# Kernel optimization log

Hardware: AMD Instinct MI355X
Metric: run time of the kernel (lower is better)

## Reference

```python
import jax, jax.numpy as jnp
import numpy as np
import math

IN_FEATURES = 512
RFF_FEATURES = 2048
OUT_FEATURES = 1000
N = 8192
RIDGE_PENALTY = 1.0
MEAN_FIELD_FACTOR = 25.0
RFF_SCALAR = math.sqrt(RFF_FEATURES / 2)  # 32.0


def _random_ortho(key, n, m):
    q, _ = jnp.linalg.qr(jax.random.normal(key, (n, m), dtype=jnp.float32))
    return q


def setup_inputs() -> dict:
    key = jax.random.key(0)
    k_d, k_w, k_norm, k_b, k_lw, k_lb, k_cov = jax.random.split(key, 7)
    D = jax.random.normal(k_d, (N, IN_FEATURES), dtype=jnp.float32)
    # RFF weight: concat of random orthonormal blocks (rff_features > in_features)
    ws = []
    dim_left = RFF_FEATURES
    kk = k_w
    while dim_left > IN_FEATURES:
        kk, sub = jax.random.split(kk)
        ws.append(_random_ortho(sub, IN_FEATURES, IN_FEATURES))
        dim_left -= IN_FEATURES
    kk, sub = jax.random.split(kk)
    ws.append(_random_ortho(sub, IN_FEATURES, dim_left))
    W = jnp.concatenate(ws, axis=1)  # [in, rff]
    feature_norm = jax.random.normal(k_norm, W.shape, dtype=jnp.float32) ** 2
    W = W * jnp.sqrt(feature_norm.sum(0))
    b = jax.random.uniform(k_b, (RFF_FEATURES,), dtype=jnp.float32) * (2.0 * math.pi)
    # logit head (nn.Linear): weight [out, rff], bias [out]
    bound = 1.0 / math.sqrt(RFF_FEATURES)
    logit_w = jax.random.uniform(k_lw, (OUT_FEATURES, RFF_FEATURES), dtype=jnp.float32,
                                 minval=-bound, maxval=bound)
    logit_b = jax.random.uniform(k_lb, (OUT_FEATURES,), dtype=jnp.float32,
                                 minval=-bound, maxval=bound)
    # positive-definite covariance buffer (stand-in for inverted precision)
    A = jax.random.normal(k_cov, (RFF_FEATURES, RFF_FEATURES), dtype=jnp.float32) * 0.01
    covariance = A @ A.T + jnp.eye(RFF_FEATURES, dtype=jnp.float32)
    return {"D": D, "W": W, "b": b, "logit_w": logit_w, "logit_b": logit_b,
            "covariance": covariance}


def reference(D, W, b, logit_w, logit_b, covariance):
    # RFF feature map: cos(D @ W + b) / rff_scalar  -> [N, rff]
    Phi = jnp.cos(D @ W + b) / RFF_SCALAR
    # linear head -> [N, out]
    pred = Phi @ logit_w.T + logit_b
    # diag(Phi @ cov @ Phi.T) * ridge computed row-wise in O(N*r^2)
    diag_cov = jnp.sum((Phi @ covariance) * Phi, axis=-1) * RIDGE_PENALTY  # [N]
    logits_scale = jnp.sqrt(1.0 + diag_cov * MEAN_FIELD_FACTOR)
    return pred / logits_scale[:, None]
```

## Files before the change

### kernel.cpp

```cpp
#include <hip/hip_runtime.h>
#include <hip/hip_fp8.h>
#include <math.h>

#define N_ROWS 8192
#define IN_F   512
#define RFF    2048
#define OUT_F  1000
#define OUT_PAD 1024
#define INV_RFF_SCALAR 0.03125f
#define MEAN_FIELD 25.0f
#define PHI_NT 24
#define PRED_NT 32

typedef __attribute__((ext_vector_type(8))) short short8;
typedef __attribute__((ext_vector_type(4))) float f32x4;
typedef __attribute__((ext_vector_type(2))) long long2v;

__device__ __forceinline__ unsigned short f32_to_bf16(float f) {
    unsigned u = __float_as_uint(f);
    unsigned r = 0x7FFFu + ((u >> 16) & 1u);
    return (unsigned short)((u + r) >> 16);
}
__device__ __forceinline__ float bf16_to_f32(unsigned short h) {
    return __uint_as_float(((unsigned)h) << 16);
}
__device__ __forceinline__ unsigned char f32_to_fp8(float x) {
    __hip_fp8_e4m3 q(x);
    return (unsigned char)q.__x;
}

__device__ __forceinline__ int perm64(int k) {
    return (k & ~63) | (((k >> 3) & 3) << 4) | (((k >> 5) & 1) << 3) | (k & 7);
}

__device__ __forceinline__ void stage_tile8(const unsigned char* __restrict__ X,
                                            int r0, int k0b, unsigned char* lds,
                                            int w, int lane) {
    #pragma unroll
    for (int h = 0; h < 4; ++h) {
        int qb = h * 256 + w * 64;
        int q = qb + lane;
        int rt = q >> 7, c = (q >> 4) & 7, r = q & 15;
        const void* g = X + (size_t)(r0 + rt * 16 + r) * RFF + k0b + c * 16;
        __builtin_amdgcn_global_load_lds(
            (const __attribute__((address_space(1))) void*)g,
            (__attribute__((address_space(3))) void*)(lds + qb * 16),
            16, 0, 0);
    }
}

__global__ __launch_bounds__(256) void conv_split_kernel(
    const float* __restrict__ X, unsigned short* __restrict__ H,
    unsigned short* __restrict__ L, int n4)
{
    int i = blockIdx.x * 256 + threadIdx.x;
    if (i >= n4) return;
    float4 v = ((const float4*)X)[i];
    ushort4 h, l;
    h.x = f32_to_bf16(v.x); l.x = f32_to_bf16(v.x - bf16_to_f32(h.x));
    h.y = f32_to_bf16(v.y); l.y = f32_to_bf16(v.y - bf16_to_f32(h.y));
    h.z = f32_to_bf16(v.z); l.z = f32_to_bf16(v.z - bf16_to_f32(h.z));
    h.w = f32_to_bf16(v.w); l.w = f32_to_bf16(v.w - bf16_to_f32(h.w));
    ((ushort4*)H)[i] = h;
    ((ushort4*)L)[i] = l;
}

__global__ __launch_bounds__(256) void conv_covu8_kernel(
    const float* __restrict__ X, unsigned char* __restrict__ O)
{
    int i = blockIdx.x * 256 + threadIdx.x;
    int base = i * 4;
    int row = base >> 11;
    int col = base & 2047;
    int bn = row >> 7, bk = col >> 7;
    float w = (bk < bn) ? 16.0f : (bk == bn ? 8.0f : 0.0f);
    float4 v = ((const float4*)X)[i];
    float w0 = (col + 0 == row) ? 0.0f : w;
    float w1 = (col + 1 == row) ? 0.0f : w;
    float w2 = (col + 2 == row) ? 0.0f : w;
    float w3 = (col + 3 == row) ? 0.0f : w;
    uchar4 o;
    o.x = f32_to_fp8(v.x * w0); o.y = f32_to_fp8(v.y * w1);
    o.z = f32_to_fp8(v.z * w2); o.w = f32_to_fp8(v.w * w3);
    *(uchar4*)(O + (size_t)row * RFF + perm64(col)) = o;
}

__global__ __launch_bounds__(256) void conv_covd_kernel(
    const float* __restrict__ X, float* __restrict__ Cd)
{
    int i = blockIdx.x * 256 + threadIdx.x;
    if (i < RFF) Cd[i] = X[(size_t)i * RFF + i];
}

__global__ __launch_bounds__(256) void conv_phi8_kernel(
    const unsigned short* __restrict__ Phi16, unsigned char* __restrict__ Phi8)
{
    int i = blockIdx.x * 256 + threadIdx.x;
    int base = i * 4;
    int row = base >> 11;
    int col = base & 2047;
    ushort4 v = ((const ushort4*)Phi16)[i];
    uchar4 o;
    o.x = f32_to_fp8(bf16_to_f32(v.x) * 32.0f);
    o.y = f32_to_fp8(bf16_to_f32(v.y) * 32.0f);
    o.z = f32_to_fp8(bf16_to_f32(v.z) * 32.0f);
    o.w = f32_to_fp8(bf16_to_f32(v.w) * 32.0f);
    *(uchar4*)(Phi8 + (size_t)row * RFF + perm64(col)) = o;
}

__global__ __launch_bounds__(256) void conv_lw_kernel(
    const float* __restrict__ Lw, unsigned short* __restrict__ O)
{
    int i = blockIdx.x * 256 + threadIdx.x;
    int base = i * 4;
    int row = base >> 11;
    ushort4 o;
    if (row < OUT_F) {
        float4 v = ((const float4*)Lw)[i];
        o.x = f32_to_bf16(v.x); o.y = f32_to_bf16(v.y);
        o.z = f32_to_bf16(v.z); o.w = f32_to_bf16(v.w);
    } else {
        o.x = o.y = o.z = o.w = 0;
    }
    ((ushort4*)O)[i] = o;
}

__global__ __launch_bounds__(256) void conv_wt_kernel(
    const float* __restrict__ W, unsigned short* __restrict__ TH,
    unsigned short* __restrict__ TL)
{
    __shared__ float tile[64][65];
    const int tid = threadIdx.x;
    const int n0 = blockIdx.x * 64;
    const int k0 = blockIdx.y * 64;
    #pragma unroll
    for (int i = 0; i < 16; ++i) {
        int e = i * 256 + tid;
        int r = e >> 6, c = e & 63;
        tile[r][c] = W[(size_t)(k0 + r) * RFF + n0 + c];
    }
    __syncthreads();
    #pragma unroll
    for (int i = 0; i < 16; ++i) {
        int e = i * 256 + tid;
        int r = e >> 6, c = e & 63;
        float v = tile[c][r];
        unsigned short h = f32_to_bf16(v);
        unsigned short l = f32_to_bf16(v - bf16_to_f32(h));
        TH[(size_t)(n0 + r) * IN_F + k0 + c] = h;
        TL[(size_t)(n0 + r) * IN_F + k0 + c] = l;
    }
}


__device__ __forceinline__ void gload16u(const void* g, unsigned short* lds) {
    __builtin_amdgcn_global_load_lds(
        (const __attribute__((address_space(1))) void*)g,
        (__attribute__((address_space(3))) void*)lds, 16, 0, 0);
}

__device__ __forceinline__ void stage_ab(const unsigned short* __restrict__ src,
                                         int stride, int r0v, int kk,
                                         unsigned short* ldsbuf,
                                         int Qa, int h, int w, int lane) {
    int q   = w * 64 + lane;
    int RT  = h * 8 + Qa * 4 + (q >> 7);
    int c   = (q >> 4) & 7, r = q & 15;
    const void* g = src + (size_t)(r0v + RT * 16 + r) * stride + kk + c * 8;
    int RTu = h * 8 + Qa * 4 + (w >> 1);
    int cu  = (w & 1) * 4;
    gload16u(g, ldsbuf + RTu * 1024 + cu * 128);
}

__device__ __forceinline__ void stageB_g(const unsigned short* __restrict__ src,
                                         int cc0, int kk, unsigned short* ldsbuf,
                                         int nh, int h, int w, int lane) {
    int q    = w * 64 + lane;
    int i    = q >> 7;
    int RTp  = (i >> 1) * 4 + nh * 2 + (i & 1);
    int c    = (q >> 4) & 7, r = q & 15;
    const void* g = src + (size_t)(cc0 + h * 128 + RTp * 16 + r) * IN_F + kk + c * 8;
    int iu   = w >> 1;
    int RTpu = (iu >> 1) * 4 + nh * 2 + (iu & 1);
    int RTu  = h * 8 + RTpu;
    int cu   = (w & 1) * 4;
    gload16u(g, ldsbuf + RTu * 1024 + cu * 128);
}

#define SB0() __builtin_amdgcn_sched_barrier(0)
#define BARRIER() do { SB0(); __builtin_amdgcn_s_barrier(); SB0(); } while (0)
#define WAITVM(N) do { asm volatile("s_waitcnt vmcnt(" #N ")"); SB0(); } while (0)


#define READ_FA(FA, mh) do {                                                  \
    _Pragma("unroll")                                                         \
    for (int i_ = 0; i_ < 4; ++i_) {                                          \
        FA[i_][0] = *(const short8*)(A + (wm * 8 + (mh) * 4 + i_) * 1024      \
                                       + quad * 128 + ln * 8);                \
        FA[i_][1] = *(const short8*)(A + (wm * 8 + (mh) * 4 + i_) * 1024      \
                                       + 512 + quad * 128 + ln * 8);          \
    } } while (0)

#define READ_FB(FB, nh) do {                                                  \
    _Pragma("unroll")                                                         \
    for (int j_ = 0; j_ < 2; ++j_) {                                          \
        FB[j_][0] = *(const short8*)(B + (wn * 4 + (nh) * 2 + j_) * 1024      \
                                       + quad * 128 + ln * 8);                \
        FB[j_][1] = *(const short8*)(B + (wn * 4 + (nh) * 2 + j_) * 1024      \
                                       + 512 + quad * 128 + ln * 8);          \
    } } while (0)

#define MFMA16(MH, NH, FA, FB) do {                                           \
    __builtin_amdgcn_s_setprio(1);                                            \
    _Pragma("unroll")                                                         \
    for (int s_ = 0; s_ < 2; ++s_)                                            \
        _Pragma("unroll")                                                     \
        for (int i_ = 0; i_ < 4; ++i_)                                        \
            _Pragma("unroll")                                                 \
            for (int j_ = 0; j_ < 2; ++j_)                                    \
                acc[(MH) * 4 + i_][(NH) * 2 + j_] =                           \
                    __builtin_amdgcn_mfma_f32_16x16x32_bf16(                  \
                        FA[i_][s_], FB[j_][s_],                               \
                        acc[(MH) * 4 + i_][(NH) * 2 + j_], 0, 0, 0);          \
    __builtin_amdgcn_s_setprio(0);                                            \
} while (0)

__global__ __launch_bounds__(512, 2) void phi_mfma8p_kernel(
    const unsigned short* __restrict__ Dh, const unsigned short* __restrict__ Dl,
    const unsigned short* __restrict__ Wth, const unsigned short* __restrict__ Wtl,
    const float* __restrict__ bias, unsigned short* __restrict__ Phi)
{
    __shared__ unsigned short ldsA[2 * 16384];
    __shared__ unsigned short ldsB[2 * 16384];
    const int tid = threadIdx.x;
    const int w = tid >> 6, lane = tid & 63;
    const int wm = w >> 2, wn = w & 3;
    const int quad = lane >> 4, ln = lane & 15;

    const int bid = blockIdx.x;
    const int xcd = bid & 7, idx = bid >> 3;
    const int rb = (xcd >> 1) * 8 + (idx & 7);
    const int cb = (xcd & 1) * 4 + (idx >> 3);
    const int r0 = rb * 256;
    const int c0 = cb * 256;

    f32x4 acc[8][4];
    #pragma unroll
    for (int i = 0; i < 8; ++i)
        #pragma unroll
        for (int j = 0; j < 4; ++j)
            acc[i][j] = (f32x4)(0.0f);

    stage_ab(Dh, IN_F, r0, 0, ldsA, 0, 0, w, lane);
    stage_ab(Dh, IN_F, r0, 0, ldsA, 0, 1, w, lane);
    stage_ab(Dh, IN_F, r0, 0, ldsA, 1, 0, w, lane);
    stage_ab(Dh, IN_F, r0, 0, ldsA, 1, 1, w, lane);
    stageB_g(Wth, c0, 0, ldsB, 0, 0, w, lane);
    stageB_g(Wth, c0, 0, ldsB, 0, 1, w, lane);
    stageB_g(Wth, c0, 0, ldsB, 1, 0, w, lane);
    stageB_g(Wth, c0, 0, ldsB, 1, 1, w, lane);
    stage_ab(Dh, IN_F, r0, 64, ldsA + 16384, 0, 0, w, lane);
    stage_ab(Dh, IN_F, r0, 64, ldsA + 16384, 0, 1, w, lane);
    stageB_g(Wth, c0, 64, ldsB + 16384, 0, 0, w, lane);
    stageB_g(Wth, c0, 64, ldsB + 16384, 0, 1, w, lane);
    WAITVM(4);
    BARRIER();

    for (int t = 0; t < PHI_NT - 1; ++t) {
        const int buf = t & 1;
        const unsigned short* A = ldsA + buf * 16384;
        const unsigned short* B = ldsB + buf * 16384;
        unsigned short* curA = ldsA + buf * 16384;
        unsigned short* curB = ldsB + buf * 16384;
        unsigned short* othA = ldsA + (buf ^ 1) * 16384;
        unsigned short* othB = ldsB + (buf ^ 1) * 16384;
        const bool has2 = (t + 2) < PHI_NT;
        const int k1 = (t + 1) * 64, k2 = (t + 2) * 64;
        const int kk1 = k1 & 511, kk2 = k2 & 511;
        const unsigned short* A1 = (k1 >= 1024) ? Dl : Dh;
        const unsigned short* B1 = (k1 >= 1024) ? Wth : (k1 >= 512 ? Wtl : Wth);
        const unsigned short* A2 = (k2 >= 1024) ? Dl : Dh;
        const unsigned short* B2 = (k2 >= 1024) ? Wth : (k2 >= 512 ? Wtl : Wth);

        short8 fa[4][2], fb0[2][2], fb1[2][2];

        READ_FA(fa, 0);
        READ_FB(fb0, 0);
        stage_ab(A1, IN_F, r0, kk1, othA, 1, 0, w, lane);
        stage_ab(A1, IN_F, r0, kk1, othA, 1, 1, w, lane);
        BARRIER();
        MFMA16(0, 0, fa, fb0);
        BARRIER();

        READ_FB(fb1, 1);
        stageB_g(B1, c0, kk1, othB, 1, 0, w, lane);
        stageB_g(B1, c0, kk1, othB, 1, 1, w, lane);
        BARRIER();
        MFMA16(0, 1, fa, fb1);
        BARRIER();

        READ_FA(fa, 1);
        if (has2) { stage_ab(A2, IN_F, r0, kk2, curA, 0, 0, w, lane);
                    stage_ab(A2, IN_F, r0, kk2, curA, 0, 1, w, lane); }
        BARRIER();
        MFMA16(1, 0, fa, fb0);
        BARRIER();

        if (has2) { stageB_g(B2, c0, kk2, curB, 0, 0, w, lane);
                    stageB_g(B2, c0, kk2, curB, 0, 1, w, lane);
                    WAITVM(4); }
        else      { WAITVM(0); }
        BARRIER();
        MFMA16(1, 1, fa, fb1);
        BARRIER();
    }

    {
        asm volatile("" ::: "memory");
        const unsigned short* A = ldsA + ((PHI_NT - 1) & 1) * 16384;
        const unsigned short* B = ldsB + ((PHI_NT - 1) & 1) * 16384;
        short8 fa[4][2], fb0[2][2], fb1[2][2];
        READ_FA(fa, 0);
        READ_FB(fb0, 0);
        READ_FB(fb1, 1);
        MFMA16(0, 0, fa, fb0);
        MFMA16(0, 1, fa, fb1);
        READ_FA(fa, 1);
        MFMA16(1, 0, fa, fb0);
        MFMA16(1, 1, fa, fb1);
    }

    float bv[4];
    #pragma unroll
    for (int nt = 0; nt < 4; ++nt)
        bv[nt] = bias[c0 + wn * 64 + nt * 16 + ln];
    #pragma unroll
    for (int mt = 0; mt < 8; ++mt)
        #pragma unroll
        for (int nt = 0; nt < 4; ++nt) {
            int col = c0 + wn * 64 + nt * 16 + ln;
            #pragma unroll
            for (int reg = 0; reg < 4; ++reg) {
                int row = r0 + wm * 128 + mt * 16 + quad * 4 + reg;
                float z = acc[mt][nt][reg] + bv[nt];
                float p = __cosf(z) * INV_RFF_SCALAR;
                Phi[(size_t)row * RFF + col] = f32_to_bf16(p);
            }
        }
}

__global__ __launch_bounds__(256, 2) void diag8_kernel(
    const unsigned char* __restrict__ Phi8, const unsigned char* __restrict__ CovU8,
    const unsigned short* __restrict__ Phi16, const float* __restrict__ Cd,
    float* __restrict__ diag)
{
    __shared__ __align__(16) unsigned char ldsA[2 * 16384];
    __shared__ __align__(16) unsigned char ldsB[2 * 16384];
    const int tid = threadIdx.x;
    const int w = tid >> 6, lane = tid & 63;
    const int wm = w >> 1, wn = w & 1;
    const int quad = lane >> 4, ln = lane & 15;
    const int J = 15 - blockIdx.x;
    const int r0 = blockIdx.y * 128;
    const int c0 = J * 128;
    const int kmax = (J + 1) * 128;

    f32x4 acc[4][4];
    #pragma unroll
    for (int i = 0; i < 4; ++i)
        #pragma unroll
        for (int j = 0; j < 4; ++j)
            acc[i][j] = (f32x4)(0.0f);

    stage_tile8(Phi8,  r0, 0, ldsA, w, lane);
    stage_tile8(CovU8, c0, 0, ldsB, w, lane);
    WAITVM(0);
    BARRIER();

    int it = 0;
    for (int k0 = 0; k0 < kmax; k0 += 128, ++it) {
        const int buf = it & 1;
        const unsigned char* A = ldsA + buf * 16384;
        const unsigned char* B = ldsB + buf * 16384;

        if (k0 + 128 < kmax) {
            stage_tile8(Phi8,  r0, k0 + 128, ldsA + (buf ^ 1) * 16384, w, lane);
            stage_tile8(CovU8, c0, k0 + 128, ldsB + (buf ^ 1) * 16384, w, lane);
        }

        __builtin_amdgcn_s_setprio(1);
        #pragma unroll
        for (int kb = 0; kb < 2; ++kb) {
            long2v fa[4], fb[4];
            #pragma unroll
            for (int t = 0; t < 4; ++t) {
                fa[t] = *(const long2v*)(A + (((wm * 4 + t) * 128 + (kb * 4 + quad) * 16 + ln) << 4));
                fb[t] = *(const long2v*)(B + (((wn * 4 + t) * 128 + (kb * 4 + quad) * 16 + ln) << 4));
            }
            #pragma unroll
            for (int mt = 0; mt < 4; ++mt)
                #pragma unroll
                for (int nt = 0; nt < 4; ++nt)
                    acc[mt][nt] = __builtin_amdgcn_mfma_f32_16x16x32_fp8_fp8(
                        fa[mt].x, fb[nt].x, acc[mt][nt], 0, 0, 0);
            #pragma unroll
            for (int mt = 0; mt < 4; ++mt)
                #pragma unroll
                for (int nt = 0; nt < 4; ++nt)
                    acc[mt][nt] = __builtin_amdgcn_mfma_f32_16x16x32_fp8_fp8(
                        fa[mt].y, fb[nt].y, acc[mt][nt], 0, 0, 0);
        }
        __builtin_amdgcn_s_setprio(0);

        WAITVM(0);
        BARRIER();
    }

    float cd[4];
    #pragma unroll
    for (int nt = 0; nt < 4; ++nt)
        cd[nt] = 256.0f * Cd[c0 + wn * 64 + nt * 16 + ln];
    #pragma unroll
    for (int mt = 0; mt < 4; ++mt) {
        float psum[4] = {0.f, 0.f, 0.f, 0.f};
        #pragma unroll
        for (int nt = 0; nt < 4; ++nt) {
            int col = c0 + wn * 64 + nt * 16 + ln;
            #pragma unroll
            for (int reg = 0; reg < 4; ++reg) {
                int row = r0 + wm * 64 + mt * 16 + quad * 4 + reg;
                float pv = bf16_to_f32(Phi16[(size_t)row * RFF + col]);
                psum[reg] = fmaf(fmaf(cd[nt], pv, acc[mt][nt][reg]), pv, psum[reg]);
            }
        }
        #pragma unroll
        for (int off = 1; off < 16; off <<= 1)
            #pragma unroll
            for (int reg = 0; reg < 4; ++reg)
                psum[reg] += __shfl_xor(psum[reg], off, 16);
        if (ln == 0) {
            #pragma unroll
            for (int reg = 0; reg < 4; ++reg) {
                int row = r0 + wm * 64 + mt * 16 + quad * 4 + reg;
                atomicAdd(&diag[row], psum[reg] * (1.0f / 256.0f));
            }
        }
    }
}

__global__ __launch_bounds__(512, 2) void pred_min2_kernel(
    const unsigned short* __restrict__ Phi, const unsigned short* __restrict__ Lw,
    const float* __restrict__ Lb, const float* __restrict__ diag,
    float* __restrict__ out)
{
    __shared__ unsigned short ldsA[2 * 16384];
    __shared__ unsigned short ldsB[2 * 8192];
    const int tid = threadIdx.x;
    const int w = tid >> 6, lane = tid & 63;
    const int wm = w >> 1, wn = w & 1;
    const int quad = lane >> 4, ln = lane & 15;

    const int bid = blockIdx.x;
    const int xcd = bid & 7, idx = bid >> 3;
    const int rb = xcd * 4 + (idx >> 3);
    const int cb = idx & 7;
    const int r0 = rb * 256;
    const int c0 = cb * 128;

    f32x4 acc[4][4];
    #pragma unroll
    for (int i = 0; i < 4; ++i)
        #pragma unroll
        for (int j = 0; j < 4; ++j)
            acc[i][j] = (f32x4)(0.0f);

    stage_ab(Phi, RFF, r0, 0, ldsA, 0, 0, w, lane);
    stage_ab(Phi, RFF, r0, 0, ldsA, 1, 0, w, lane);
    stage_ab(Phi, RFF, r0, 0, ldsA, 0, 1, w, lane);
    stage_ab(Phi, RFF, r0, 0, ldsA, 1, 1, w, lane);
    stage_ab(Lw,  RFF, c0, 0, ldsB, 0, 0, w, lane);
    stage_ab(Lw,  RFF, c0, 0, ldsB, 1, 0, w, lane);
    WAITVM(0);
    BARRIER();

    for (int t = 0; t < PRED_NT; ++t) {
        const int buf = t & 1;
        const unsigned short* A = ldsA + buf * 16384;
        const unsigned short* B = ldsB + buf * 8192;

        if (t + 1 < PRED_NT) {
            const int kk = (t + 1) * 64;
            unsigned short* nA = ldsA + (buf ^ 1) * 16384;
            unsigned short* nB = ldsB + (buf ^ 1) * 8192;
            stage_ab(Phi, RFF, r0, kk, nA, 0, 0, w, lane);
            stage_ab(Phi, RFF, r0, kk, nA, 1, 0, w, lane);
            stage_ab(Phi, RFF, r0, kk, nA, 0, 1, w, lane);
            stage_ab(Phi, RFF, r0, kk, nA, 1, 1, w, lane);
            stage_ab(Lw,  RFF, c0, kk, nB, 0, 0, w, lane);
            stage_ab(Lw,  RFF, c0, kk, nB, 1, 0, w, lane);
        }

        short8 fa[4][2], fb[4][2];
        #pragma unroll
        for (int i_ = 0; i_ < 4; ++i_) {
            fa[i_][0] = *(const short8*)(A + (wm * 4 + i_) * 1024 + quad * 128 + ln * 8);
            fa[i_][1] = *(const short8*)(A + (wm * 4 + i_) * 1024 + 512 + quad * 128 + ln * 8);
        }
        #pragma unroll
        for (int j_ = 0; j_ < 4; ++j_) {
            fb[j_][0] = *(const short8*)(B + (wn * 4 + j_) * 1024 + quad * 128 + ln * 8);
            fb[j_][1] = *(const short8*)(B + (wn * 4 + j_) * 1024 + 512 + quad * 128 + ln * 8);
        }
        __builtin_amdgcn_s_setprio(1);
        #pragma unroll
        for (int s_ = 0; s_ < 2; ++s_)
            #pragma unroll
            for (int i_ = 0; i_ < 4; ++i_)
                #pragma unroll
                for (int j_ = 0; j_ < 4; ++j_)
                    acc[i_][j_] = __builtin_amdgcn_mfma_f32_16x16x32_bf16(
                        fa[i_][s_], fb[j_][s_], acc[i_][j_], 0, 0, 0);
        __builtin_amdgcn_s_setprio(0);

        WAITVM(0);
        BARRIER();
    }

    #pragma unroll
    for (int mt = 0; mt < 4; ++mt) {
        float s[4];
        #pragma unroll
        for (int reg = 0; reg < 4; ++reg) {
            int row = r0 + wm * 64 + mt * 16 + quad * 4 + reg;
            s[reg] = 1.0f / sqrtf(1.0f + MEAN_FIELD * diag[row]);
        }
        #pragma unroll
        for (int nt = 0; nt < 4; ++nt) {
            int col = c0 + wn * 64 + nt * 16 + ln;
            if (col < OUT_F) {
                float bv = Lb[col];
                #pragma unroll
                for (int reg = 0; reg < 4; ++reg) {
                    int row = r0 + wm * 64 + mt * 16 + quad * 4 + reg;
                    out[(size_t)row * OUT_F + col] = (acc[mt][nt][reg] + bv) * s[reg];
                }
            }
        }
    }
}

extern "C" void kernel_launch(void* const* d_in, const int* in_sizes, int n_in,
                              void* d_out, int out_size, void* d_ws, size_t ws_size,
                              hipStream_t stream) {
    const float* D    = (const float*)d_in[0];
    const float* W    = (const float*)d_in[1];
    const float* bias = (const float*)d_in[2];
    const float* Lw   = (const float*)d_in[3];
    const float* Lb   = (const float*)d_in[4];
    const float* cov  = (const float*)d_in[5];
    float* out = (float*)d_out;

    char* p = (char*)d_ws;
    unsigned short* Phi16 = (unsigned short*)p;  p += (size_t)N_ROWS * RFF * 2;
    unsigned char*  Phi8  = (unsigned char*)p;
    unsigned short* Dh    = (unsigned short*)p;  p += (size_t)N_ROWS * IN_F * 2;
    unsigned short* Dl    = (unsigned short*)p;  p += (size_t)N_ROWS * IN_F * 2;
    unsigned short* Wth   = (unsigned short*)p;  p += (size_t)RFF * IN_F * 2;
    unsigned short* Wtl   = (unsigned short*)p;  p += (size_t)RFF * IN_F * 2;
    unsigned short* Lw16  = (unsigned short*)p;  p += (size_t)OUT_PAD * RFF * 2;
    unsigned char*  CovU8 = (unsigned char*)p;
    float*          Cd    = (float*)(p + (size_t)RFF * RFF);
    p += (size_t)RFF * RFF * 2;
    float* diag           = (float*)p;

    hipMemsetAsync(diag, 0, N_ROWS * sizeof(float), stream);

    dim3 blk(256);
    conv_split_kernel<<<dim3((N_ROWS * IN_F / 4 + 255) / 256), blk, 0, stream>>>(D, Dh, Dl, N_ROWS * IN_F / 4);
    conv_wt_kernel<<<dim3(RFF / 64, IN_F / 64), blk, 0, stream>>>(W, Wth, Wtl);
    conv_lw_kernel<<<dim3(OUT_PAD * RFF / 4 / 256), blk, 0, stream>>>(Lw, Lw16);
    conv_covu8_kernel<<<dim3(RFF * RFF / 4 / 256), blk, 0, stream>>>(cov, CovU8);
    conv_covd_kernel<<<dim3(RFF / 256), blk, 0, stream>>>(cov, Cd);

    phi_mfma8p_kernel<<<dim3(256), dim3(512), 0, stream>>>(Dh, Dl, Wth, Wtl, bias, Phi16);
    conv_phi8_kernel<<<dim3(N_ROWS * RFF / 4 / 256), blk, 0, stream>>>(Phi16, Phi8);

    diag8_kernel<<<dim3(16, N_ROWS / 128), blk, 0, stream>>>(Phi8, CovU8, Phi16, Cd, diag);
    pred_min2_kernel<<<dim3(256), dim3(512), 0, stream>>>(Phi16, Lw16, Lb, diag, out);
}
```

Measured before the change: 317.3 us.

## Drop LDS staging in diag and pred GEMMs, load fragments directly from global

Removes the double-buffered LDS staging and barriers from the fp8 diag kernel and the bf16 pred kernel, so each wave loads its MFMA fragments straight from global memory and relies on cache for reuse. The pred kernel moves to 256-thread blocks on 128-row tiles with twice as many blocks, and diag raises its occupancy hint. The covariance diagonal extraction is folded into the fp8 conversion kernel, which saves one launch. Direct global loads give up the explicit reuse and latency hiding that LDS double-buffering provided, so the GEMMs may stall on memory.

```diff
diff --git a/kernel.cpp b/kernel.cpp
--- a/kernel.cpp
+++ b/kernel.cpp
@@ -10,7 +10,6 @@
 #define INV_RFF_SCALAR 0.03125f
 #define MEAN_FIELD 25.0f
 #define PHI_NT 24
-#define PRED_NT 32
 
 typedef __attribute__((ext_vector_type(8))) short short8;
 typedef __attribute__((ext_vector_type(4))) float f32x4;
@@ -31,22 +30,6 @@
 
 __device__ __forceinline__ int perm64(int k) {
     return (k & ~63) | (((k >> 3) & 3) << 4) | (((k >> 5) & 1) << 3) | (k & 7);
-}
-
-__device__ __forceinline__ void stage_tile8(const unsigned char* __restrict__ X,
-                                            int r0, int k0b, unsigned char* lds,
-                                            int w, int lane) {
-    #pragma unroll
-    for (int h = 0; h < 4; ++h) {
-        int qb = h * 256 + w * 64;
-        int q = qb + lane;
-        int rt = q >> 7, c = (q >> 4) & 7, r = q & 15;
-        const void* g = X + (size_t)(r0 + rt * 16 + r) * RFF + k0b + c * 16;
-        __builtin_amdgcn_global_load_lds(
-            (const __attribute__((address_space(1))) void*)g,
-            (__attribute__((address_space(3))) void*)(lds + qb * 16),
-            16, 0, 0);
-    }
 }
 
 __global__ __launch_bounds__(256) void conv_split_kernel(
@@ -66,7 +49,8 @@
 }
 
 __global__ __launch_bounds__(256) void conv_covu8_kernel(
-    const float* __restrict__ X, unsigned char* __restrict__ O)
+    const float* __restrict__ X, unsigned char* __restrict__ O,
+    float* __restrict__ Cd)
 {
     int i = blockIdx.x * 256 + threadIdx.x;
     int base = i * 4;
@@ -75,21 +59,17 @@
     int bn = row >> 7, bk = col >> 7;
     float w = (bk < bn) ? 16.0f : (bk == bn ? 8.0f : 0.0f);
     float4 v = ((const float4*)X)[i];
-    float w0 = (col + 0 == row) ? 0.0f : w;
-    float w1 = (col + 1 == row) ? 0.0f : w;
-    float w2 = (col + 2 == row) ? 0.0f : w;
-    float w3 = (col + 3 == row) ? 0.0f : w;
+    float vv[4] = {v.x, v.y, v.z, v.w};
+    float wj[4];
+    #pragma unroll
+    for (int j = 0; j < 4; ++j) {
+        if (col + j == row) { wj[j] = 0.0f; Cd[row] = vv[j]; }
+        else wj[j] = w;
+    }
     uchar4 o;
-    o.x = f32_to_fp8(v.x * w0); o.y = f32_to_fp8(v.y * w1);
-    o.z = f32_to_fp8(v.z * w2); o.w = f32_to_fp8(v.w * w3);
+    o.x = f32_to_fp8(vv[0] * wj[0]); o.y = f32_to_fp8(vv[1] * wj[1]);
+    o.z = f32_to_fp8(vv[2] * wj[2]); o.w = f32_to_fp8(vv[3] * wj[3]);
     *(uchar4*)(O + (size_t)row * RFF + perm64(col)) = o;
-}
-
-__global__ __launch_bounds__(256) void conv_covd_kernel(
-    const float* __restrict__ X, float* __restrict__ Cd)
-{
-    int i = blockIdx.x * 256 + threadIdx.x;
-    if (i < RFF) Cd[i] = X[(size_t)i * RFF + i];
 }
 
 __global__ __launch_bounds__(256) void conv_phi8_kernel(
@@ -349,13 +329,11 @@
         }
 }
 
-__global__ __launch_bounds__(256, 2) void diag8_kernel(
+__global__ __launch_bounds__(256, 3) void diag8_kernel(
     const unsigned char* __restrict__ Phi8, const unsigned char* __restrict__ CovU8,
     const unsigned short* __restrict__ Phi16, const float* __restrict__ Cd,
     float* __restrict__ diag)
 {
-    __shared__ __align__(16) unsigned char ldsA[2 * 16384];
-    __shared__ __align__(16) unsigned char ldsB[2 * 16384];
     const int tid = threadIdx.x;
     const int w = tid >> 6, lane = tid & 63;
     const int wm = w >> 1, wn = w & 1;
@@ -365,6 +343,9 @@
     const int c0 = J * 128;
     const int kmax = (J + 1) * 128;
 
+    const unsigned char* aB = Phi8  + (size_t)(r0 + wm * 64 + ln) * RFF + quad * 16;
+    const unsigned char* bB = CovU8 + (size_t)(c0 + wn * 64 + ln) * RFF + quad * 16;
+
     f32x4 acc[4][4];
     #pragma unroll
     for (int i = 0; i < 4; ++i)
@@ -372,30 +353,14 @@
         for (int j = 0; j < 4; ++j)
             acc[i][j] = (f32x4)(0.0f);
 
-    stage_tile8(Phi8,  r0, 0, ldsA, w, lane);
-    stage_tile8(CovU8, c0, 0, ldsB, w, lane);
-    WAITVM(0);
-    BARRIER();
-
-    int it = 0;
-    for (int k0 = 0; k0 < kmax; k0 += 128, ++it) {
-        const int buf = it & 1;
-        const unsigned char* A = ldsA + buf * 16384;
-        const unsigned char* B = ldsB + buf * 16384;
-
-        if (k0 + 128 < kmax) {
-            stage_tile8(Phi8,  r0, k0 + 128, ldsA + (buf ^ 1) * 16384, w, lane);
-            stage_tile8(CovU8, c0, k0 + 128, ldsB + (buf ^ 1) * 16384, w, lane);
-        }
-
-        __builtin_amdgcn_s_setprio(1);
+    for (int k0 = 0; k0 < kmax; k0 += 128) {
         #pragma unroll
         for (int kb = 0; kb < 2; ++kb) {
             long2v fa[4], fb[4];
             #pragma unroll
             for (int t = 0; t < 4; ++t) {
-                fa[t] = *(const long2v*)(A + (((wm * 4 + t) * 128 + (kb * 4 + quad) * 16 + ln) << 4));
-                fb[t] = *(const long2v*)(B + (((wn * 4 + t) * 128 + (kb * 4 + quad) * 16 + ln) << 4));
+                fa[t] = *(const long2v*)(aB + (size_t)t * 16 * RFF + kb * 64 + k0);
+                fb[t] = *(const long2v*)(bB + (size_t)t * 16 * RFF + kb * 64 + k0);
             }
             #pragma unroll
             for (int mt = 0; mt < 4; ++mt)
@@ -410,10 +375,6 @@
                     acc[mt][nt] = __builtin_amdgcn_mfma_f32_16x16x32_fp8_fp8(
                         fa[mt].y, fb[nt].y, acc[mt][nt], 0, 0, 0);
         }
-        __builtin_amdgcn_s_setprio(0);
-
-        WAITVM(0);
-        BARRIER();
     }
 
     float cd[4];
@@ -448,13 +409,11 @@
     }
 }
 
-__global__ __launch_bounds__(512, 2) void pred_min2_kernel(
+__global__ __launch_bounds__(256, 2) void pred_direct_kernel(
     const unsigned short* __restrict__ Phi, const unsigned short* __restrict__ Lw,
     const float* __restrict__ Lb, const float* __restrict__ diag,
     float* __restrict__ out)
 {
-    __shared__ unsigned short ldsA[2 * 16384];
-    __shared__ unsigned short ldsB[2 * 8192];
     const int tid = threadIdx.x;
     const int w = tid >> 6, lane = tid & 63;
     const int wm = w >> 1, wn = w & 1;
@@ -462,10 +421,13 @@
 
     const int bid = blockIdx.x;
     const int xcd = bid & 7, idx = bid >> 3;
-    const int rb = xcd * 4 + (idx >> 3);
+    const int rb = xcd * 8 + (idx >> 3);
     const int cb = idx & 7;
-    const int r0 = rb * 256;
+    const int r0 = rb * 128;
     const int c0 = cb * 128;
+
+    const unsigned short* aB = Phi + (size_t)(r0 + wm * 64 + ln) * RFF + quad * 8;
+    const unsigned short* bB = Lw  + (size_t)(c0 + wn * 64 + ln) * RFF + quad * 8;
 
     f32x4 acc[4][4];
     #pragma unroll
@@ -474,44 +436,19 @@
         for (int j = 0; j < 4; ++j)
             acc[i][j] = (f32x4)(0.0f);
 
-    stage_ab(Phi, RFF, r0, 0, ldsA, 0, 0, w, lane);
-    stage_ab(Phi, RFF, r0, 0, ldsA, 1, 0, w, lane);
-    stage_ab(Phi, RFF, r0, 0, ldsA, 0, 1, w, lane);
-    stage_ab(Phi, RFF, r0, 0, ldsA, 1, 1, w, lane);
-    stage_ab(Lw,  RFF, c0, 0, ldsB, 0, 0, w, lane);
-    stage_ab(Lw,  RFF, c0, 0, ldsB, 1, 0, w, lane);
-    WAITVM(0);
-    BARRIER();
-
-    for (int t = 0; t < PRED_NT; ++t) {
-        const int buf = t & 1;
-        const unsigned short* A = ldsA + buf * 16384;
-        const unsigned short* B = ldsB + buf * 8192;
-
-        if (t + 1 < PRED_NT) {
-            const int kk = (t + 1) * 64;
-            unsigned short* nA = ldsA + (buf ^ 1) * 16384;
-            unsigned short* nB = ldsB + (buf ^ 1) * 8192;
-            stage_ab(Phi, RFF, r0, kk, nA, 0, 0, w, lane);
-            stage_ab(Phi, RFF, r0, kk, nA, 1, 0, w, lane);
-            stage_ab(Phi, RFF, r0, kk, nA, 0, 1, w, lane);
-            stage_ab(Phi, RFF, r0, kk, nA, 1, 1, w, lane);
-            stage_ab(Lw,  RFF, c0, kk, nB, 0, 0, w, lane);
-            stage_ab(Lw,  RFF, c0, kk, nB, 1, 0, w, lane);
-        }
-
+    #pragma unroll 2
+    for (int k0 = 0; k0 < RFF; k0 += 64) {
         short8 fa[4][2], fb[4][2];
         #pragma unroll
         for (int i_ = 0; i_ < 4; ++i_) {
-            fa[i_][0] = *(const short8*)(A + (wm * 4 + i_) * 1024 + quad * 128 + ln * 8);
-            fa[i_][1] = *(const short8*)(A + (wm * 4 + i_) * 1024 + 512 + quad * 128 + ln * 8);
+            fa[i_][0] = *(const short8*)(aB + (size_t)i_ * 16 * RFF + k0);
+            fa[i_][1] = *(const short8*)(aB + (size_t)i_ * 16 * RFF + k0 + 32);
         }
         #pragma unroll
         for (int j_ = 0; j_ < 4; ++j_) {
-            fb[j_][0] = *(const short8*)(B + (wn * 4 + j_) * 1024 + quad * 128 + ln * 8);
-            fb[j_][1] = *(const short8*)(B + (wn * 4 + j_) * 1024 + 512 + quad * 128 + ln * 8);
-        }
-        __builtin_amdgcn_s_setprio(1);
+            fb[j_][0] = *(const short8*)(bB + (size_t)j_ * 16 * RFF + k0);
+            fb[j_][1] = *(const short8*)(bB + (size_t)j_ * 16 * RFF + k0 + 32);
+        }
         #pragma unroll
         for (int s_ = 0; s_ < 2; ++s_)
             #pragma unroll
@@ -520,10 +457,6 @@
                 for (int j_ = 0; j_ < 4; ++j_)
                     acc[i_][j_] = __builtin_amdgcn_mfma_f32_16x16x32_bf16(
                         fa[i_][s_], fb[j_][s_], acc[i_][j_], 0, 0, 0);
-        __builtin_amdgcn_s_setprio(0);
-
-        WAITVM(0);
-        BARRIER();
     }
 
     #pragma unroll
@@ -579,12 +512,11 @@
     conv_split_kernel<<<dim3((N_ROWS * IN_F / 4 + 255) / 256), blk, 0, stream>>>(D, Dh, Dl, N_ROWS * IN_F / 4);
     conv_wt_kernel<<<dim3(RFF / 64, IN_F / 64), blk, 0, stream>>>(W, Wth, Wtl);
     conv_lw_kernel<<<dim3(OUT_PAD * RFF / 4 / 256), blk, 0, stream>>>(Lw, Lw16);
-    conv_covu8_kernel<<<dim3(RFF * RFF / 4 / 256), blk, 0, stream>>>(cov, CovU8);
-    conv_covd_kernel<<<dim3(RFF / 256), blk, 0, stream>>>(cov, Cd);
+    conv_covu8_kernel<<<dim3(RFF * RFF / 4 / 256), blk, 0, stream>>>(cov, CovU8, Cd);
 
     phi_mfma8p_kernel<<<dim3(256), dim3(512), 0, stream>>>(Dh, Dl, Wth, Wtl, bias, Phi16);
     conv_phi8_kernel<<<dim3(N_ROWS * RFF / 4 / 256), blk, 0, stream>>>(Phi16, Phi8);
 
     diag8_kernel<<<dim3(16, N_ROWS / 128), blk, 0, stream>>>(Phi8, CovU8, Phi16, Cd, diag);
-    pred_min2_kernel<<<dim3(256), dim3(512), 0, stream>>>(Phi16, Lw16, Lb, diag, out);
-}
+    pred_direct_kernel<<<dim3(512), blk, 0, stream>>>(Phi16, Lw16, Lb, diag, out);
+}
```

After: 419.5 us. +32.2%, slower.
